# Performance work log

Measured on AMD Instinct MI355X. Metric: run time of the kernel, lower is better.

Reference implementation:

```python
import jax, jax.numpy as jnp
import numpy as np

B, S, D, H = 4, 1500, 1280, 20
HD = D // H  # 64

def setup_inputs() -> dict:
    key = jax.random.key(0)
    ks = jax.random.split(key, 8)
    scale = 1.0 / np.sqrt(D)
    return {
        "hidden_states": jax.random.normal(ks[0], (B, S, D), dtype=jnp.float32),
        "attention_mask": jnp.zeros((B, 1, S, S), dtype=jnp.float32),
        "q_w": jax.random.normal(ks[1], (D, D), dtype=jnp.float32) * scale,
        "q_b": jax.random.normal(ks[2], (D,), dtype=jnp.float32) * 0.02,
        "k_w": jax.random.normal(ks[3], (D, D), dtype=jnp.float32) * scale,
        "v_w": jax.random.normal(ks[4], (D, D), dtype=jnp.float32) * scale,
        "v_b": jax.random.normal(ks[5], (D,), dtype=jnp.float32) * 0.02,
        "o_w": jax.random.normal(ks[6], (D, D), dtype=jnp.float32) * scale,
        "o_b": jax.random.normal(ks[7], (D,), dtype=jnp.float32) * 0.02,
    }

def reference(hidden_states, attention_mask, q_w, q_b, k_w, v_w, v_b, o_w, o_b):
    bsz, seq_len, d_model = hidden_states.shape
    scaling = HD ** (-0.5)
    # Projections (k_proj has NO bias, matching the module)
    q = hidden_states @ q_w + q_b
    k = hidden_states @ k_w
    v = hidden_states @ v_w + v_b
    # [B, H, S, HD]
    q = q.reshape(bsz, seq_len, H, HD).transpose(0, 2, 1, 3)
    k = k.reshape(bsz, seq_len, H, HD).transpose(0, 2, 1, 3)
    v = v.reshape(bsz, seq_len, H, HD).transpose(0, 2, 1, 3)
    scores = jnp.einsum("bhqd,bhkd->bhqk", q, k) * scaling
    scores = scores + attention_mask
    attn = jax.nn.softmax(scores.astype(jnp.float32), axis=-1).astype(q.dtype)
    out = jnp.einsum("bhqk,bhkd->bhqd", attn, v)
    out = out.transpose(0, 2, 1, 3).reshape(bsz, seq_len, d_model)
    return out @ o_w + o_b
```

## Files before the change

kernel.cpp:

```cpp
#include <hip/hip_runtime.h>
#include <hip/hip_bf16.h>
#include <cstddef>

#define B_   4
#define S_   1500
#define D_   1280
#define H_   20
#define HD_  64
#define M_   (B_*S_)
#define SPAD 1536
#define BIGNEG (-1e30f)
#define LOG2E 1.44269504088896340736f
#define KVB  64
#define NTA  24

typedef short bf16x8 __attribute__((ext_vector_type(8)));
typedef float f32x4 __attribute__((ext_vector_type(4)));
typedef unsigned short u16;
typedef u16 u16x8 __attribute__((ext_vector_type(8)));
typedef unsigned int u32x4v __attribute__((ext_vector_type(4)));

#define MFMA __builtin_amdgcn_mfma_f32_16x16x32_bf16

__device__ __forceinline__ u16 f2bf(float f) {
  union { float f; unsigned u; } x; x.f = f;
  unsigned r = (x.u + 0x7fffu + ((x.u >> 16) & 1u)) >> 16;
  return (u16)r;
}

__device__ __forceinline__ unsigned cvtpk(float a, float b) {
  unsigned r;
  asm volatile("v_cvt_pk_bf16_f32 %0, %1, %2" : "=v"(r) : "v"(a), "v"(b));
  return r;
}

__device__ __forceinline__ void gl_lds16(const u16* g, u16* l) {
  typedef __attribute__((address_space(1))) const unsigned GU;
  typedef __attribute__((address_space(3))) unsigned LU;
  __builtin_amdgcn_global_load_lds((GU*)g, (LU*)l, 16, 0, 0);
}

__global__ __launch_bounds__(256) void k_conv(const float* __restrict__ X, u16* __restrict__ Y) {
  size_t i = (size_t)blockIdx.x * 256 + threadIdx.x;
  const float4* p = (const float4*)(X + i * 8);
  float4 a = p[0], b = p[1];
  u16x8 v;
  v[0]=f2bf(a.x); v[1]=f2bf(a.y); v[2]=f2bf(a.z); v[3]=f2bf(a.w);
  v[4]=f2bf(b.x); v[5]=f2bf(b.y); v[6]=f2bf(b.z); v[7]=f2bf(b.w);
  *(u16x8*)(Y + i * 8) = v;
}

__global__ __launch_bounds__(256) void k_mscan(const float* __restrict__ m, int* __restrict__ flag) {
  const size_t tot = (size_t)B_ * S_ * S_;
  size_t i = ((size_t)blockIdx.x * 256 + threadIdx.x) * 4;
  size_t stride = (size_t)gridDim.x * 256 * 4;
  for (; i < tot; i += stride) {
    float4 v = *(const float4*)(m + i);
    if (v.x != 0.f || v.y != 0.f || v.z != 0.f || v.w != 0.f) {
      int b = (int)(i / ((size_t)S_ * S_));
      atomicOr(&flag[b], 1);
    }
  }
}

__global__ __launch_bounds__(256) void k_trans4(const float* __restrict__ qw,
                                                const float* __restrict__ kw,
                                                const float* __restrict__ vw,
                                                const float* __restrict__ ow,
                                                u16* __restrict__ Wt) {
  const float* W = (blockIdx.z == 0) ? qw : (blockIdx.z == 1) ? kw
                   : (blockIdx.z == 2) ? vw : ow;
  u16* dst = Wt + (size_t)blockIdx.z * D_ * D_;
  __shared__ float t[32][33];
  int n0 = blockIdx.x * 32, k0 = blockIdx.y * 32;
  int tx = threadIdx.x & 31, ty = threadIdx.x >> 5;
  #pragma unroll
  for (int i = ty; i < 32; i += 8) t[i][tx] = W[(size_t)(k0 + i) * D_ + n0 + tx];
  __syncthreads();
  #pragma unroll
  for (int i = ty; i < 32; i += 8) dst[(size_t)(n0 + i) * D_ + k0 + tx] = f2bf(t[tx][i]);
}

__global__ __launch_bounds__(256) void k_vtrans(const u16* __restrict__ Vb, u16* __restrict__ Vt) {
  __shared__ u16 t[128][72];
  int bh = blockIdx.x, b = bh / H_, h = bh % H_;
  int s0 = blockIdx.y * 128;
  int tid = threadIdx.x;
  #pragma unroll
  for (int r = 0; r < 4; r++) {
    int sl = r * 32 + (tid >> 3);
    int s = s0 + sl; if (s > S_ - 1) s = S_ - 1;
    bf16x8 v = *(const bf16x8*)(Vb + ((size_t)(b * S_ + s)) * D_ + h * HD_ + (tid & 7) * 8);
    *(bf16x8*)&t[sl][(tid & 7) * 8] = v;
  }
  __syncthreads();
  #pragma unroll
  for (int r = 0; r < 4; r++) {
    int d = r * 16 + (tid >> 4);
    int ss = (tid & 15) * 8;
    u16x8 o;
    #pragma unroll
    for (int q = 0; q < 8; q++) {
      int sl = ss + q;
      int kk = ((sl >> 4) & 3) * 4 + (sl & 3) + ((sl >> 2) & 3) * 16 + (sl & 64);
      o[q] = t[kk][d];
    }
    *(u16x8*)(Vt + ((size_t)bh * HD_ + d) * SPAD + s0 + ss) = o;
  }
}

__global__ __launch_bounds__(256) void k_gemmqkv(const u16* __restrict__ A,
                                                 const u16* __restrict__ Wt,
                                                 const float* __restrict__ q_b,
                                                 const float* __restrict__ v_b,
                                                 u16* __restrict__ Qb) {
  int p = blockIdx.x;
  int gg = p & 7;
  int idx = p >> 3;
  int y = idx / 6;
  int x = gg * 6 + idx % 6;
  if (x >= 47) return;

  __shared__ u16 As[128 * 64];
  __shared__ u16 Bs[128 * 64];
  int tid = threadIdx.x;
  int lane = tid & 63;
  int wv = tid >> 6;
  int l16 = lane & 15, lg = lane >> 4;
  int wr = wv >> 1, wc = wv & 1;
  int m0 = x * 128;
  int n0g = y * 128;
  int sel = y / 10;
  int nloc = n0g - sel * 1280;

  int srow = tid >> 3;
  int csw = ((tid & 7) ^ (srow & 7)) * 8;
  const u16* asrc = A + csw;
  const u16* bsrc = Wt + csw;
  int dbase = wv * 8 * 64;

  f32x4 acc[4][4] = {};

#define STAGEG(tt) do {                                                  \
    int kk0 = (tt) * 64;                                                 \
    _Pragma("unroll")                                                    \
    for (int c = 0; c < 4; c++) {                                        \
      int row = srow + c * 32;                                           \
      int ar = m0 + row; if (ar > M_ - 1) ar = M_ - 1;                   \
      gl_lds16(asrc + (size_t)ar * D_ + kk0, &As[0] + dbase + c * 2048); \
      gl_lds16(bsrc + (size_t)(n0g + row) * D_ + kk0,                    \
               &Bs[0] + dbase + c * 2048);                               \
    }                                                                    \
  } while (0)

  for (int t = 0; t < 20; t++) {
    STAGEG(t);
    __syncthreads();
    #pragma unroll
    for (int kk = 0; kk < 2; kk++) {
      int pcol = ((kk * 4 + lg) ^ (l16 & 7)) * 8;
      bf16x8 af[4], bf[4];
      #pragma unroll
      for (int m = 0; m < 4; m++)
        af[m] = *(const bf16x8*)&As[(wr * 64 + m * 16 + l16) * 64 + pcol];
      #pragma unroll
      for (int n = 0; n < 4; n++)
        bf[n] = *(const bf16x8*)&Bs[(wc * 64 + n * 16 + l16) * 64 + pcol];
      __builtin_amdgcn_s_setprio(1);
      #pragma unroll
      for (int m = 0; m < 4; m++)
        #pragma unroll
        for (int n = 0; n < 4; n++)
          acc[m][n] = MFMA(af[m], bf[n], acc[m][n], 0, 0, 0);
      __builtin_amdgcn_s_setprio(0);
    }
    __syncthreads();
  }
#undef STAGEG

  const float* bias = (sel == 0) ? q_b : v_b;
  float scl = (sel == 0) ? (0.125f * LOG2E) : 1.0f;
  u16* outb = Qb + (size_t)sel * ((size_t)M_ * D_);

  #pragma unroll
  for (int m = 0; m < 4; m++) {
    int row0 = m0 + wr * 64 + m * 16 + lg * 4;
    #pragma unroll
    for (int n = 0; n < 4; n++) {
      int colL = nloc + wc * 64 + n * 16 + l16;
      float bv = (sel == 1) ? 0.0f : bias[colL];
      #pragma unroll
      for (int j = 0; j < 4; j++) {
        int row = row0 + j;
        if (row < M_) {
          float v = (acc[m][n][j] + bv) * scl;
          outb[(size_t)row * D_ + colL] = f2bf(v);
        }
      }
    }
  }
}

__global__ __launch_bounds__(256) void k_gemmo(const u16* __restrict__ A,
                                               const u16* __restrict__ Wt,
                                               const float* __restrict__ bias,
                                               float* __restrict__ outp) {
  int p = blockIdx.x;
  int gg = p & 7;
  int idx = p >> 3;
  int y = idx / 6;
  int x = gg * 6 + idx % 6;
  if (x >= 47) return;

  __shared__ u16 As[128 * 64];
  __shared__ u16 Bs[128 * 64];
  int tid = threadIdx.x;
  int lane = tid & 63;
  int wv = tid >> 6;
  int l16 = lane & 15, lg = lane >> 4;
  int wr = wv >> 1, wc = wv & 1;
  int m0 = x * 128, n0 = y * 128;

  int srow = tid >> 3;
  int csw = ((tid & 7) ^ (srow & 7)) * 8;
  const u16* asrc = A + csw;
  const u16* bsrc = Wt + csw;
  int dbase = wv * 8 * 64;

  f32x4 acc[4][4] = {};

#define STAGEG(tt) do {                                                  \
    int kk0 = (tt) * 64;                                                 \
    _Pragma("unroll")                                                    \
    for (int c = 0; c < 4; c++) {                                        \
      int row = srow + c * 32;                                           \
      int ar = m0 + row; if (ar > M_ - 1) ar = M_ - 1;                   \
      gl_lds16(asrc + (size_t)ar * D_ + kk0, &As[0] + dbase + c * 2048); \
      gl_lds16(bsrc + (size_t)(n0 + row) * D_ + kk0,                     \
               &Bs[0] + dbase + c * 2048);                               \
    }                                                                    \
  } while (0)

  for (int t = 0; t < 20; t++) {
    STAGEG(t);
    __syncthreads();
    #pragma unroll
    for (int kk = 0; kk < 2; kk++) {
      int pcol = ((kk * 4 + lg) ^ (l16 & 7)) * 8;
      bf16x8 af[4], bf[4];
      #pragma unroll
      for (int m = 0; m < 4; m++)
        af[m] = *(const bf16x8*)&As[(wr * 64 + m * 16 + l16) * 64 + pcol];
      #pragma unroll
      for (int n = 0; n < 4; n++)
        bf[n] = *(const bf16x8*)&Bs[(wc * 64 + n * 16 + l16) * 64 + pcol];
      __builtin_amdgcn_s_setprio(1);
      #pragma unroll
      for (int m = 0; m < 4; m++)
        #pragma unroll
        for (int n = 0; n < 4; n++)
          acc[m][n] = MFMA(af[m], bf[n], acc[m][n], 0, 0, 0);
      __builtin_amdgcn_s_setprio(0);
    }
    __syncthreads();
  }
#undef STAGEG

  #pragma unroll
  for (int m = 0; m < 4; m++) {
    int row0 = m0 + wr * 64 + m * 16 + lg * 4;
    #pragma unroll
    for (int n = 0; n < 4; n++) {
      int col = n0 + wc * 64 + n * 16 + l16;
      float bv = bias[col];
      #pragma unroll
      for (int j = 0; j < 4; j++) {
        int row = row0 + j;
        if (row < M_) outp[(size_t)row * D_ + col] = acc[m][n][j] + bv;
      }
    }
  }
}

__global__ __launch_bounds__(256) void k_attn(const u16* __restrict__ Qb,
                                              const u16* __restrict__ Kb,
                                              const u16* __restrict__ Vt,
                                              const float* __restrict__ mask,
                                              const int* __restrict__ mflag,
                                              u16* __restrict__ Ctx) {
  __shared__ u16 Kl[2][64 * 64];
  __shared__ u16 Vl[2][64 * 64];

  int p = blockIdx.x;
  int L = (p & 7) * 120 + (p >> 3);
  int h = L % 20;
  int g = L / 20;
  int b = g / 12;
  int xq = g % 12;
  int bh = b * H_ + h;
  int um = mflag[b];

  int tid = threadIdx.x;
  int lane = tid & 63, wv = tid >> 6;
  int l16 = lane & 15, lg = lane >> 4;
  int qw0 = xq * 128 + wv * 16;

  int qr0 = qw0 + l16;      if (qr0 > S_ - 1) qr0 = S_ - 1;
  int qr1 = qw0 + 64 + l16; if (qr1 > S_ - 1) qr1 = S_ - 1;
  const u16* qp0 = Qb + ((size_t)(b * S_ + qr0)) * D_ + h * HD_ + lg * 8;
  const u16* qp1 = Qb + ((size_t)(b * S_ + qr1)) * D_ + h * HD_ + lg * 8;
  bf16x8 aq00 = *(const bf16x8*)(qp0);
  bf16x8 aq01 = *(const bf16x8*)(qp0 + 32);
  bf16x8 aq10 = *(const bf16x8*)(qp1);
  bf16x8 aq11 = *(const bf16x8*)(qp1 + 32);
  const float* mrow0 = mask + (size_t)b * S_ * S_ + (size_t)qr0 * S_;
  const float* mrow1 = mask + (size_t)b * S_ * S_ + (size_t)qr1 * S_;

  int sr0 = wv * 16 + (lane >> 3);
  int csw = ((lane & 7) ^ (lane >> 3)) * 8;
  const u16* ksrc = Kb + (size_t)b * S_ * D_ + h * HD_ + csw;
  const u16* vsrc0 = Vt + ((size_t)bh * HD_ + sr0) * SPAD + csw;
  const u16* vsrc1 = vsrc0 + 8 * SPAD;

  float m0_ = BIGNEG, l0_ = 0.0f, m1_ = BIGNEG, l1_ = 0.0f;
  f32x4 acc0[4] = {}, acc1[4] = {};
  const f32x4 zf = {0, 0, 0, 0};

#define STAGE(k0s, bufb) do {                                          \
    int key0_ = (k0s) + sr0;     if (key0_ > S_ - 1) key0_ = S_ - 1;   \
    int key1_ = key0_ + 8;       if (key1_ > S_ - 1) key1_ = S_ - 1;   \
    u16* kd_ = &Kl[bufb][0] + wv * 1024;                               \
    u16* vd_ = &Vl[bufb][0] + wv * 1024;                               \
    gl_lds16(ksrc + (size_t)key0_ * D_, kd_);                          \
    gl_lds16(ksrc + (size_t)key1_ * D_, kd_ + 512);                    \
    gl_lds16(vsrc0 + (k0s), vd_);                                      \
    gl_lds16(vsrc1 + (k0s), vd_ + 512);                                \
  } while (0)

#define SMX(sv, mm, ll, accv) do {                                     \
    float t0 = fmaxf(fmaxf(sv[0][0], sv[0][1]), fmaxf(sv[0][2], sv[0][3])); \
    float t1 = fmaxf(fmaxf(sv[1][0], sv[1][1]), fmaxf(sv[1][2], sv[1][3])); \
    float t2 = fmaxf(fmaxf(sv[2][0], sv[2][1]), fmaxf(sv[2][2], sv[2][3])); \
    float t3 = fmaxf(fmaxf(sv[3][0], sv[3][1]), fmaxf(sv[3][2], sv[3][3])); \
    float rmax = fmaxf(fmaxf(t0, t1), fmaxf(t2, t3));                  \
    rmax = fmaxf(rmax, __shfl_xor(rmax, 16));                          \
    rmax = fmaxf(rmax, __shfl_xor(rmax, 32));                          \
    float mn = fmaxf(mm, rmax);                                        \
    if (!__all(mn - mm <= 8.0f)) {                                     \
      float c = __builtin_amdgcn_exp2f(mm - mn);                       \
      mm = mn; ll *= c;                                                \
      _Pragma("unroll")                                                \
      for (int j = 0; j < 4; j++) {                                    \
        float cj = __shfl(c, lg * 4 + j);                              \
        accv[0][j] *= cj; accv[1][j] *= cj;                            \
        accv[2][j] *= cj; accv[3][j] *= cj;                            \
      }                                                                \
    }                                                                  \
    _Pragma("unroll")                                                  \
    for (int sub = 0; sub < 4; sub++)                                  \
      _Pragma("unroll")                                                \
      for (int j = 0; j < 4; j++)                                      \
        sv[sub][j] = __builtin_amdgcn_exp2f(sv[sub][j] - mm);          \
    float a0 = (sv[0][0] + sv[0][1]) + (sv[0][2] + sv[0][3]);          \
    float a1 = (sv[1][0] + sv[1][1]) + (sv[1][2] + sv[1][3]);          \
    float a2 = (sv[2][0] + sv[2][1]) + (sv[2][2] + sv[2][3]);          \
    float a3 = (sv[3][0] + sv[3][1]) + (sv[3][2] + sv[3][3]);          \
    ll += (a0 + a1) + (a2 + a3);                                       \
  } while (0)

#define COMPUTE(curb, k0_, LASTV) do {                                 \
    const u16* KlC = &Kl[curb][0];                                     \
    const u16* VlC = &Vl[curb][0];                                     \
    f32x4 s0[4], s1[4];                                                \
    __builtin_amdgcn_s_setprio(1);                                     \
    _Pragma("unroll")                                                  \
    for (int sub = 0; sub < 4; sub++) {                                \
      const u16* kb = KlC + (sub * 16 + l16) * 64;                     \
      bf16x8 kf0 = *(const bf16x8*)(kb + ((lg     ^ (l16 & 7)) * 8));  \
      bf16x8 kf1 = *(const bf16x8*)(kb + (((4+lg) ^ (l16 & 7)) * 8));  \
      s0[sub] = MFMA(kf0, aq00, zf, 0, 0, 0);                          \
      s0[sub] = MFMA(kf1, aq01, s0[sub], 0, 0, 0);                     \
      s1[sub] = MFMA(kf0, aq10, zf, 0, 0, 0);                          \
      s1[sub] = MFMA(kf1, aq11, s1[sub], 0, 0, 0);                     \
    }                                                                  \
    __builtin_amdgcn_s_setprio(0);                                     \
    if (um) {                                                          \
      _Pragma("unroll")                                                \
      for (int sub = 0; sub < 4; sub++) {                              \
        int mc = (k0_) + sub * 16 + lg * 4;                            \
        if (mc > S_ - 4) mc = S_ - 4;                                  \
        float4 mv0 = *(const float4*)(mrow0 + mc);                     \
        float4 mv1 = *(const float4*)(mrow1 + mc);                     \
        s0[sub][0] = fmaf(mv0.x, LOG2E, s0[sub][0]);                   \
        s0[sub][1] = fmaf(mv0.y, LOG2E, s0[sub][1]);                   \
        s0[sub][2] = fmaf(mv0.z, LOG2E, s0[sub][2]);                   \
        s0[sub][3] = fmaf(mv0.w, LOG2E, s0[sub][3]);                   \
        s1[sub][0] = fmaf(mv1.x, LOG2E, s1[sub][0]);                   \
        s1[sub][1] = fmaf(mv1.y, LOG2E, s1[sub][1]);                   \
        s1[sub][2] = fmaf(mv1.z, LOG2E, s1[sub][2]);                   \
        s1[sub][3] = fmaf(mv1.w, LOG2E, s1[sub][3]);                   \
      }                                                                \
    }                                                                  \
    if (LASTV) {                                                       \
      _Pragma("unroll")                                                \
      for (int sub = 0; sub < 4; sub++) {                              \
        int kb_ = (k0_) + sub * 16 + lg * 4;                           \
        _Pragma("unroll")                                              \
        for (int j = 0; j < 4; j++)                                    \
          if (kb_ + j >= S_) { s0[sub][j] = BIGNEG; s1[sub][j] = BIGNEG; } \
      }                                                                \
    }                                                                  \
    SMX(s0, m0_, l0_, acc0);                                           \
    union { u32x4v u; bf16x8 bf; } pA0, pA1;                           \
    pA0.u[0] = cvtpk(s0[0][0], s0[0][1]); pA0.u[1] = cvtpk(s0[0][2], s0[0][3]); \
    pA0.u[2] = cvtpk(s0[1][0], s0[1][1]); pA0.u[3] = cvtpk(s0[1][2], s0[1][3]); \
    pA1.u[0] = cvtpk(s0[2][0], s0[2][1]); pA1.u[1] = cvtpk(s0[2][2], s0[2][3]); \
    pA1.u[2] = cvtpk(s0[3][0], s0[3][1]); pA1.u[3] = cvtpk(s0[3][2], s0[3][3]); \
    SMX(s1, m1_, l1_, acc1);                                           \
    union { u32x4v u; bf16x8 bf; } pB0, pB1;                           \
    pB0.u[0] = cvtpk(s1[0][0], s1[0][1]); pB0.u[1] = cvtpk(s1[0][2], s1[0][3]); \
    pB0.u[2] = cvtpk(s1[1][0], s1[1][1]); pB0.u[3] = cvtpk(s1[1][2], s1[1][3]); \
    pB1.u[0] = cvtpk(s1[2][0], s1[2][1]); pB1.u[1] = cvtpk(s1[2][2], s1[2][3]); \
    pB1.u[2] = cvtpk(s1[3][0], s1[3][1]); pB1.u[3] = cvtpk(s1[3][2], s1[3][3]); \
    __builtin_amdgcn_s_setprio(1);                                     \
    _Pragma("unroll")                                                  \
    for (int n = 0; n < 4; n++) {                                      \
      const u16* vb = VlC + (n * 16 + l16) * 64;                       \
      bf16x8 bv0 = *(const bf16x8*)(vb + (((lg*2  ) ^ (l16 & 7)) * 8));\
      bf16x8 bv1 = *(const bf16x8*)(vb + (((lg*2+1) ^ (l16 & 7)) * 8));\
      acc0[n] = MFMA(pA0.bf, bv0, acc0[n], 0, 0, 0);                   \
      acc0[n] = MFMA(pA1.bf, bv1, acc0[n], 0, 0, 0);                   \
      acc1[n] = MFMA(pB0.bf, bv0, acc1[n], 0, 0, 0);                   \
      acc1[n] = MFMA(pB1.bf, bv1, acc1[n], 0, 0, 0);                   \
    }                                                                  \
    __builtin_amdgcn_s_setprio(0);                                     \
  } while (0)

  STAGE(0, 0);

  for (int t = 0; t < NTA - 1; t++) {
    int k0 = t * KVB;
    __builtin_amdgcn_s_barrier();
    asm volatile("" ::: "memory");
    STAGE(k0 + KVB, (t + 1) & 1);
    asm volatile("s_waitcnt vmcnt(4)" ::: "memory");
    __builtin_amdgcn_s_barrier();
    asm volatile("" ::: "memory");
    COMPUTE(t & 1, k0, false);
  }
  {
    const int k0 = (NTA - 1) * KVB;
    __builtin_amdgcn_s_barrier();
    asm volatile("s_waitcnt vmcnt(0)" ::: "memory");
    __builtin_amdgcn_s_barrier();
    asm volatile("" ::: "memory");
    COMPUTE((NTA - 1) & 1, k0, true);
  }

  l0_ += __shfl_xor(l0_, 16);
  l0_ += __shfl_xor(l0_, 32);
  l1_ += __shfl_xor(l1_, 16);
  l1_ += __shfl_xor(l1_, 32);
  float inv0 = 1.0f / l0_;
  float inv1 = 1.0f / l1_;
  #pragma unroll
  for (int j = 0; j < 4; j++) {
    float ivj0 = __shfl(inv0, lg * 4 + j);
    float ivj1 = __shfl(inv1, lg * 4 + j);
    int row0 = qw0 + lg * 4 + j;
    int row1 = row0 + 64;
    if (row0 < S_) {
      #pragma unroll
      for (int n = 0; n < 4; n++)
        Ctx[((size_t)(b * S_ + row0)) * D_ + h * HD_ + n * 16 + l16] = f2bf(acc0[n][j] * ivj0);
    }
    if (row1 < S_) {
      #pragma unroll
      for (int n = 0; n < 4; n++)
        Ctx[((size_t)(b * S_ + row1)) * D_ + h * HD_ + n * 16 + l16] = f2bf(acc1[n][j] * ivj1);
    }
  }
#undef STAGE
#undef SMX
#undef COMPUTE
}

extern "C" void kernel_launch(void* const* d_in, const int* in_sizes, int n_in,
                              void* d_out, int out_size, void* d_ws, size_t ws_size,
                              hipStream_t stream) {
  const float* hs   = (const float*)d_in[0];
  const float* mask = (const float*)d_in[1];
  const float* q_w  = (const float*)d_in[2];
  const float* q_b  = (const float*)d_in[3];
  const float* k_w  = (const float*)d_in[4];
  const float* v_w  = (const float*)d_in[5];
  const float* v_b  = (const float*)d_in[6];
  const float* o_w  = (const float*)d_in[7];
  const float* o_b  = (const float*)d_in[8];
  float* out = (float*)d_out;

  char* w = (char*)d_ws;
  const size_t XD = (size_t)M_ * D_;
  const size_t WD = (size_t)D_ * D_;
  u16* Xb  = (u16*)(w);                 w += XD * 2;
  u16* Wtq = (u16*)(w);                 w += WD * 2;
  u16* Wtk = (u16*)(w);                 w += WD * 2;
  u16* Wtv = (u16*)(w);                 w += WD * 2;
  u16* Wto = (u16*)(w);                 w += WD * 2;
  u16* Qb  = (u16*)(w);                 w += XD * 2;
  u16* Kb  = (u16*)(w);                 w += XD * 2;
  u16* Vb  = (u16*)(w);                 w += XD * 2;
  u16* Vt  = (u16*)(w);                 w += (size_t)B_ * H_ * HD_ * SPAD * 2;
  int* mflag = (int*)(w);               w += 4 * sizeof(int);
  u16* Ctx = Xb;
  (void)Wtk; (void)Wtv;

  hipMemsetAsync(mflag, 0, 4 * sizeof(int), stream);
  k_mscan<<<dim3(2048), dim3(256), 0, stream>>>(mask, mflag);

  k_conv<<<dim3(3750), dim3(256), 0, stream>>>(hs, Xb);
  k_trans4<<<dim3(40, 40, 4), dim3(256), 0, stream>>>(q_w, k_w, v_w, o_w, Wtq);

  k_gemmqkv<<<dim3(1440), dim3(256), 0, stream>>>(Xb, Wtq, q_b, v_b, Qb);
  k_vtrans<<<dim3(80, 12), dim3(256), 0, stream>>>(Vb, Vt);

  k_attn<<<dim3(960), dim3(256), 0, stream>>>(Qb, Kb, Vt, mask, mflag, Ctx);

  k_gemmo<<<dim3(480), dim3(256), 0, stream>>>(Ctx, Wto, o_b, out);
}
```

Measured before the change: 226.7 us.

## Fuse V transpose into QKV GEMM epilogue and mask scan into conversion kernel

The separate V-transpose kernel is removed. The QKV GEMM epilogue now writes V directly into the permuted, padded Vt layout that attention consumes. The mask-scan kernel is folded into the input-conversion kernel as extra blocks, saving one launch. In exchange, V is written with scattered 2-byte stores, and the padding columns of Vt (positions past the sequence length) are no longer filled, so they may hold stale data.

```diff
diff --git a/kernel.cpp b/kernel.cpp
--- a/kernel.cpp
+++ b/kernel.cpp
@@ -40,25 +40,26 @@
   __builtin_amdgcn_global_load_lds((GU*)g, (LU*)l, 16, 0, 0);
 }
 
-__global__ __launch_bounds__(256) void k_conv(const float* __restrict__ X, u16* __restrict__ Y) {
-  size_t i = (size_t)blockIdx.x * 256 + threadIdx.x;
-  const float4* p = (const float4*)(X + i * 8);
-  float4 a = p[0], b = p[1];
-  u16x8 v;
-  v[0]=f2bf(a.x); v[1]=f2bf(a.y); v[2]=f2bf(a.z); v[3]=f2bf(a.w);
-  v[4]=f2bf(b.x); v[5]=f2bf(b.y); v[6]=f2bf(b.z); v[7]=f2bf(b.w);
-  *(u16x8*)(Y + i * 8) = v;
-}
-
-__global__ __launch_bounds__(256) void k_mscan(const float* __restrict__ m, int* __restrict__ flag) {
-  const size_t tot = (size_t)B_ * S_ * S_;
-  size_t i = ((size_t)blockIdx.x * 256 + threadIdx.x) * 4;
-  size_t stride = (size_t)gridDim.x * 256 * 4;
-  for (; i < tot; i += stride) {
-    float4 v = *(const float4*)(m + i);
-    if (v.x != 0.f || v.y != 0.f || v.z != 0.f || v.w != 0.f) {
-      int b = (int)(i / ((size_t)S_ * S_));
-      atomicOr(&flag[b], 1);
+__global__ __launch_bounds__(256) void k_conv(const float* __restrict__ X, u16* __restrict__ Y,
+                                              const float* __restrict__ msk, int* __restrict__ flag) {
+  if (blockIdx.x < 3750) {
+    size_t i = (size_t)blockIdx.x * 256 + threadIdx.x;
+    const float4* p = (const float4*)(X + i * 8);
+    float4 a = p[0], b = p[1];
+    u16x8 v;
+    v[0]=f2bf(a.x); v[1]=f2bf(a.y); v[2]=f2bf(a.z); v[3]=f2bf(a.w);
+    v[4]=f2bf(b.x); v[5]=f2bf(b.y); v[6]=f2bf(b.z); v[7]=f2bf(b.w);
+    *(u16x8*)(Y + i * 8) = v;
+  } else {
+    const size_t tot = (size_t)B_ * S_ * S_;
+    size_t i = ((size_t)(blockIdx.x - 3750) * 256 + threadIdx.x) * 4;
+    size_t stride = (size_t)1024 * 256 * 4;
+    for (; i < tot; i += stride) {
+      float4 v = *(const float4*)(msk + i);
+      if (v.x != 0.f || v.y != 0.f || v.z != 0.f || v.w != 0.f) {
+        int b = (int)(i / ((size_t)S_ * S_));
+        atomicOr(&flag[b], 1);
+      }
     }
   }
 }
@@ -81,39 +82,12 @@
   for (int i = ty; i < 32; i += 8) dst[(size_t)(n0 + i) * D_ + k0 + tx] = f2bf(t[tx][i]);
 }
 
-__global__ __launch_bounds__(256) void k_vtrans(const u16* __restrict__ Vb, u16* __restrict__ Vt) {
-  __shared__ u16 t[128][72];
-  int bh = blockIdx.x, b = bh / H_, h = bh % H_;
-  int s0 = blockIdx.y * 128;
-  int tid = threadIdx.x;
-  #pragma unroll
-  for (int r = 0; r < 4; r++) {
-    int sl = r * 32 + (tid >> 3);
-    int s = s0 + sl; if (s > S_ - 1) s = S_ - 1;
-    bf16x8 v = *(const bf16x8*)(Vb + ((size_t)(b * S_ + s)) * D_ + h * HD_ + (tid & 7) * 8);
-    *(bf16x8*)&t[sl][(tid & 7) * 8] = v;
-  }
-  __syncthreads();
-  #pragma unroll
-  for (int r = 0; r < 4; r++) {
-    int d = r * 16 + (tid >> 4);
-    int ss = (tid & 15) * 8;
-    u16x8 o;
-    #pragma unroll
-    for (int q = 0; q < 8; q++) {
-      int sl = ss + q;
-      int kk = ((sl >> 4) & 3) * 4 + (sl & 3) + ((sl >> 2) & 3) * 16 + (sl & 64);
-      o[q] = t[kk][d];
-    }
-    *(u16x8*)(Vt + ((size_t)bh * HD_ + d) * SPAD + s0 + ss) = o;
-  }
-}
-
 __global__ __launch_bounds__(256) void k_gemmqkv(const u16* __restrict__ A,
                                                  const u16* __restrict__ Wt,
                                                  const float* __restrict__ q_b,
                                                  const float* __restrict__ v_b,
-                                                 u16* __restrict__ Qb) {
+                                                 u16* __restrict__ Qb,
+                                                 u16* __restrict__ Vt) {
   int p = blockIdx.x;
   int gg = p & 7;
   int idx = p >> 3;
@@ -194,7 +168,16 @@
         int row = row0 + j;
         if (row < M_) {
           float v = (acc[m][n][j] + bv) * scl;
-          outb[(size_t)row * D_ + colL] = f2bf(v);
+          if (sel == 2) {
+            int bb = row / S_;
+            int sloc = row - bb * S_;
+            int hh = colL >> 6, dd = colL & 63;
+            int k = sloc & 63;
+            int pos = ((k >> 2) & 3) * 16 + (k >> 4) * 4 + (k & 3);
+            Vt[(((size_t)(bb * H_ + hh)) * HD_ + dd) * SPAD + (sloc >> 6) * 64 + pos] = f2bf(v);
+          } else {
+            outb[(size_t)row * D_ + colL] = f2bf(v);
+          }
         }
       }
     }
@@ -513,16 +496,13 @@
   u16* Vt  = (u16*)(w);                 w += (size_t)B_ * H_ * HD_ * SPAD * 2;
   int* mflag = (int*)(w);               w += 4 * sizeof(int);
   u16* Ctx = Xb;
-  (void)Wtk; (void)Wtv;
+  (void)Wtk; (void)Wtv; (void)Vb;
 
   hipMemsetAsync(mflag, 0, 4 * sizeof(int), stream);
-  k_mscan<<<dim3(2048), dim3(256), 0, stream>>>(mask, mflag);
-
-  k_conv<<<dim3(3750), dim3(256), 0, stream>>>(hs, Xb);
+  k_conv<<<dim3(3750 + 1024), dim3(256), 0, stream>>>(hs, Xb, mask, mflag);
   k_trans4<<<dim3(40, 40, 4), dim3(256), 0, stream>>>(q_w, k_w, v_w, o_w, Wtq);
 
-  k_gemmqkv<<<dim3(1440), dim3(256), 0, stream>>>(Xb, Wtq, q_b, v_b, Qb);
-  k_vtrans<<<dim3(80, 12), dim3(256), 0, stream>>>(Vb, Vt);
+  k_gemmqkv<<<dim3(1440), dim3(256), 0, stream>>>(Xb, Wtq, q_b, v_b, Qb, Vt);
 
   k_attn<<<dim3(960), dim3(256), 0, stream>>>(Qb, Kb, Vt, mask, mflag, Ctx);
 
```

Result: slower. 233.8 us (+3.2%).
